# Performance work log

Measured on AMD Instinct MI355X. Metric: run time of the kernel, lower is better.

## Reference

```python
import jax, jax.numpy as jnp
import numpy as np

B, N, F_IN, F_OUT = 8, 2048, 128, 64
ALPHA = 0.2  # LeakyReLU negative slope
NEG_INF = -9e15


def setup_inputs() -> dict:
    key = jax.random.key(0)
    k1, k2, k3, k4 = jax.random.split(key, 4)
    h = jax.random.normal(k1, (B, N, F_IN), dtype=jnp.float32)
    adj = jax.random.randint(k2, (B, N, N), 0, 2, dtype=jnp.int32)
    # xavier_uniform with gain=1.414 approximated by scaled normals (values are arbitrary params)
    W = jax.random.normal(k3, (F_IN, F_OUT), dtype=jnp.float32) * (1.414 * np.sqrt(2.0 / (F_IN + F_OUT)))
    a = jax.random.normal(k4, (2 * F_OUT, 1), dtype=jnp.float32) * (1.414 * np.sqrt(2.0 / (2 * F_OUT + 1)))
    return {"h": h, "adj": adj, "W": W, "a": a}


def reference(h, adj, W, a):
    # Wh: [B, N, F_out]
    Wh = jnp.einsum('bnf,fo->bno', h, W)
    Fo = W.shape[1]
    a1 = a[:Fo, 0]   # [F_out]
    a2 = a[Fo:, 0]   # [F_out]
    # e[b,i,j] = leakyrelu(Wh[b,i]@a1 + Wh[b,j]@a2)  (== cat(Wh_i,Wh_j)@a, same math, no N^2*2F blowup)
    e1 = jnp.einsum('bno,o->bn', Wh, a1)  # [B, N]
    e2 = jnp.einsum('bno,o->bn', Wh, a2)  # [B, N]
    e = e1[:, :, None] + e2[:, None, :]   # [B, N, N]
    e = jnp.where(e > 0, e, ALPHA * e)    # LeakyReLU
    e = jnp.where(adj > 0, e, NEG_INF)    # mask non-edges
    attention = jax.nn.softmax(e, axis=-1)
    # dropout is identity in inference mode (deterministic reference)
    h_prime = jnp.einsum('bij,bjo->bio', attention, Wh)  # [B, N, F_out]
    return jax.nn.elu(h_prime)  # concat=True branch
```

## Files before the change

### kernel.cpp

```cpp
#include <hip/hip_runtime.h>
#include <hip/hip_bf16.h>

#define BB 8
#define NN 2048
#define FIN 128
#define FO 64
#define ALPHA 0.2f

typedef __attribute__((ext_vector_type(8))) short bf16x8;
typedef __attribute__((ext_vector_type(4))) float f32x4;
typedef __attribute__((ext_vector_type(4))) int i32x4;

typedef __attribute__((address_space(1))) const void gvoid;
typedef __attribute__((address_space(3))) void lvoid;

__device__ inline void gl_lds16(const void* g, void* l) {
    __builtin_amdgcn_global_load_lds((gvoid*)g, (lvoid*)l, 16, 0, 0);
}

__device__ inline short f2bf(float x) {
    unsigned u = __float_as_uint(x);
    u += 0x7fffu + ((u >> 16) & 1u);
    return (short)(u >> 16);
}

__global__ __launch_bounds__(256) void wh_kernel(
    const float* __restrict__ h, const float* __restrict__ W,
    const float* __restrict__ a, float* __restrict__ e1, float* __restrict__ e2,
    short* __restrict__ whF)
{
    __shared__ float hs[32][FIN];
    const int r0 = blockIdx.x * 32;
    const int t = threadIdx.x;
    const float4* hsrc = (const float4*)(h + (size_t)r0 * FIN);
    float4* hdst = (float4*)(&hs[0][0]);
#pragma unroll
    for (int k = 0; k < 4; k++) hdst[t + 256 * k] = hsrc[t + 256 * k];
    __syncthreads();

    const int o = t & 63;
    const int wv = t >> 6;
    float acc[8];
#pragma unroll
    for (int rr = 0; rr < 8; rr++) acc[rr] = 0.f;

    for (int f = 0; f < FIN; f += 4) {
        const float w0 = W[(f + 0) * FO + o];
        const float w1 = W[(f + 1) * FO + o];
        const float w2 = W[(f + 2) * FO + o];
        const float w3 = W[(f + 3) * FO + o];
#pragma unroll
        for (int rr = 0; rr < 8; rr++) {
            float4 hv = *(const float4*)&hs[wv * 8 + rr][f];
            acc[rr] = fmaf(hv.x, w0, acc[rr]);
            acc[rr] = fmaf(hv.y, w1, acc[rr]);
            acc[rr] = fmaf(hv.z, w2, acc[rr]);
            acc[rr] = fmaf(hv.w, w3, acc[rr]);
        }
    }

    const int b   = r0 / NN;
    const int ib0 = r0 - b * NN;
    const int ibb = ib0 + wv * 8;
    const int jc  = ibb >> 5;
    const int qq  = (ibb >> 3) & 3;
    const int ot  = o >> 4, mm = o & 15;
    const int L   = mm + qq * 16;
    bf16x8 frag;
#pragma unroll
    for (int rr = 0; rr < 8; rr++) frag[rr] = f2bf(acc[rr]);
    *(bf16x8*)(whF + ((((size_t)(b * 64 + jc) * 4 + ot) * 64 + L) * 8)) = frag;

    const float a1 = a[o], a2 = a[FO + o];
#pragma unroll
    for (int rr = 0; rr < 8; rr++) {
        float v1 = acc[rr] * a1, v2 = acc[rr] * a2;
#pragma unroll
        for (int msk = 32; msk >= 1; msk >>= 1) {
            v1 += __shfl_xor(v1, msk, 64);
            v2 += __shfl_xor(v2, msk, 64);
        }
        if (o == 0) { e1[r0 + wv * 8 + rr] = v1; e2[r0 + wv * 8 + rr] = v2; }
    }
}

__global__ __launch_bounds__(256) void e2max_kernel(
    const float* __restrict__ e2, float* __restrict__ e2max)
{
    const int b = blockIdx.x;
    const int t = threadIdx.x;
    float m = -1e30f;
    for (int j = t; j < NN; j += 256) m = fmaxf(m, e2[b * NN + j]);
#pragma unroll
    for (int k = 32; k >= 1; k >>= 1) m = fmaxf(m, __shfl_xor(m, k, 64));
    __shared__ float red[4];
    if ((t & 63) == 0) red[t >> 6] = m;
    __syncthreads();
    if (t == 0) e2max[b] = fmaxf(fmaxf(red[0], red[1]), fmaxf(red[2], red[3]));
}

struct SMemS { int adj[16][260]; float e2[256]; };
struct SMemC { float comb[4][16][64]; float lsum[4][16]; };
union SMemU { SMemS s; SMemC c; };

__global__ __launch_bounds__(256) void attn_kernel(
    const int* __restrict__ adj, const float* __restrict__ e1,
    const float* __restrict__ e2, const float* __restrict__ e2max,
    const short* __restrict__ whF, float* __restrict__ out)
{
    __shared__ SMemU sm;
    const int t = threadIdx.x, w = t >> 6, lane = t & 63;
    const int m = lane & 15, q = lane >> 4;
    const int blk = blockIdx.x;
    const int b  = blk >> 7;
    const int i0 = (blk & 127) * 16;
    const int i  = i0 + m;

    const float e1v = e1[b * NN + i];
    float mi = e1v + e2max[b];
    mi = mi > 0.f ? mi : ALPHA * mi;

    const short* whFb = whF + (size_t)b * (64 * 4 * 64 * 8);
    const int* arow0 = adj + ((size_t)(b * NN + i0)) * NN + lane * 4;
    const float* e2g = e2 + b * NN + lane * 4;

    f32x4 acc0 = {0.f,0.f,0.f,0.f}, acc1 = acc0, acc2 = acc0, acc3 = acc0;
    float lsum = 0.f;

    for (int j0 = 0; j0 < NN; j0 += 256) {
#pragma unroll
        for (int k = 0; k < 4; k++) {
            const int r = w * 4 + k;
            gl_lds16(arow0 + (size_t)r * NN + j0, &sm.s.adj[r][0]);
        }
        if (w == 0) gl_lds16(e2g + j0, &sm.s.e2[0]);
        __syncthreads();

#pragma unroll
        for (int s2 = 0; s2 < 2; s2++) {
            const int col = w * 64 + s2 * 32 + q * 8;
            i32x4 a0 = *(const i32x4*)&sm.s.adj[m][col];
            i32x4 a1 = *(const i32x4*)&sm.s.adj[m][col + 4];
            f32x4 ev0 = *(const f32x4*)&sm.s.e2[col];
            f32x4 ev1 = *(const f32x4*)&sm.s.e2[col + 4];

            bf16x8 af;
#pragma unroll
            for (int jj = 0; jj < 8; jj++) {
                const int   av  = (jj < 4) ? a0[jj]      : a1[jj - 4];
                const float e2j = (jj < 4) ? ev0[jj]     : ev1[jj - 4];
                float e = e1v + e2j;
                e = e > 0.f ? e : ALPHA * e;
                const float pe = (av > 0) ? __expf(e - mi) : 0.f;
                lsum += pe;
                af[jj] = f2bf(pe);
            }

            const int jc = (j0 + w * 64 + s2 * 32) >> 5;
            const short* bfp = whFb + (size_t)jc * 2048 + lane * 8;
            bf16x8 b0 = *(const bf16x8*)(bfp);
            bf16x8 b1 = *(const bf16x8*)(bfp + 512);
            bf16x8 b2 = *(const bf16x8*)(bfp + 1024);
            bf16x8 b3 = *(const bf16x8*)(bfp + 1536);

            acc0 = __builtin_amdgcn_mfma_f32_16x16x32_bf16(af, b0, acc0, 0, 0, 0);
            acc1 = __builtin_amdgcn_mfma_f32_16x16x32_bf16(af, b1, acc1, 0, 0, 0);
            acc2 = __builtin_amdgcn_mfma_f32_16x16x32_bf16(af, b2, acc2, 0, 0, 0);
            acc3 = __builtin_amdgcn_mfma_f32_16x16x32_bf16(af, b3, acc3, 0, 0, 0);
        }
        __syncthreads();
    }

    lsum += __shfl_xor(lsum, 16, 64);
    lsum += __shfl_xor(lsum, 32, 64);
    if (q == 0) sm.c.lsum[w][m] = lsum;
#pragma unroll
    for (int ot = 0; ot < 4; ot++) {
        f32x4 av = (ot == 0) ? acc0 : (ot == 1) ? acc1 : (ot == 2) ? acc2 : acc3;
#pragma unroll
        for (int reg = 0; reg < 4; reg++)
            sm.c.comb[w][q * 4 + reg][ot * 16 + m] = av[reg];
    }
    __syncthreads();

    const int row = t >> 4, c0 = (t & 15) * 4;
    f32x4 sum = *(const f32x4*)&sm.c.comb[0][row][c0];
#pragma unroll
    for (int ww = 1; ww < 4; ww++) {
        f32x4 sv = *(const f32x4*)&sm.c.comb[ww][row][c0];
        sum.x += sv.x; sum.y += sv.y; sum.z += sv.z; sum.w += sv.w;
    }
    float l = sm.c.lsum[0][row] + sm.c.lsum[1][row] + sm.c.lsum[2][row] + sm.c.lsum[3][row];
    l = fmaxf(l, 1e-30f);
    const float rl = 1.f / l;
    float vr[4] = { sum.x * rl, sum.y * rl, sum.z * rl, sum.w * rl };
    f32x4 res;
#pragma unroll
    for (int kk = 0; kk < 4; kk++)
        res[kk] = vr[kk] > 0.f ? vr[kk] : (__expf(vr[kk]) - 1.f);
    *(f32x4*)&out[((size_t)(b * NN + i0 + row)) * FO + c0] = res;
}

extern "C" void kernel_launch(void* const* d_in, const int* in_sizes, int n_in,
                              void* d_out, int out_size, void* d_ws, size_t ws_size,
                              hipStream_t stream) {
    const float* h   = (const float*)d_in[0];
    const int*   adj = (const int*)d_in[1];
    const float* W   = (const float*)d_in[2];
    const float* a   = (const float*)d_in[3];
    float* out = (float*)d_out;

    char* ws = (char*)d_ws;
    short* whF = (short*)ws;
    size_t off = (size_t)BB * 64 * 4 * 64 * 8 * sizeof(short);
    float* e1  = (float*)(ws + off);  off += (size_t)BB * NN * 4;
    float* e2  = (float*)(ws + off);  off += (size_t)BB * NN * 4;
    float* e2m = (float*)(ws + off);

    wh_kernel<<<(BB * NN) / 32, 256, 0, stream>>>(h, W, a, e1, e2, whF);
    e2max_kernel<<<BB, 256, 0, stream>>>(e2, e2m);
    attn_kernel<<<BB * (NN / 16), 256, 0, stream>>>(adj, e1, e2, e2m, whF, out);
}
```

Baseline: 216.6 us.

## Double-buffer adjacency tiles, prefetch operands to registers, fold e2 max into wh kernel

The attention kernel now double-buffers the adjacency tile in LDS and issues the next tile's global-to-LDS load before computing the current one, using manual vmcnt waits and raw barriers. The Wh fragments and e2 values are read straight into registers instead of staging e2 through LDS. The separate e2max reduction kernel is replaced by an order-preserving atomicMax in wh_kernel plus a tiny init kernel, and wh_kernel reads h directly from global instead of through LDS. This aims to hide adjacency load latency behind the exp/MFMA work. In exchange the hand-written waitcnt counts are fragile, and the extra LDS buffer plus the occupancy hint may affect occupancy.

```diff
diff --git a/kernel.cpp b/kernel.cpp
--- a/kernel.cpp
+++ b/kernel.cpp
@@ -24,22 +24,30 @@
     return (short)(u >> 16);
 }
 
+__device__ inline unsigned f2ord(float f) {
+    unsigned u = __float_as_uint(f);
+    return (u & 0x80000000u) ? ~u : (u | 0x80000000u);
+}
+__device__ inline float ord2f(unsigned v) {
+    return __uint_as_float((v & 0x80000000u) ? (v & 0x7fffffffu) : ~v);
+}
+
+__global__ void init_kernel(unsigned* __restrict__ e2m) {
+    if (threadIdx.x < BB) e2m[threadIdx.x] = 0u;
+}
+
 __global__ __launch_bounds__(256) void wh_kernel(
     const float* __restrict__ h, const float* __restrict__ W,
     const float* __restrict__ a, float* __restrict__ e1, float* __restrict__ e2,
-    short* __restrict__ whF)
+    unsigned* __restrict__ e2m, short* __restrict__ whF)
 {
-    __shared__ float hs[32][FIN];
+    const int t  = threadIdx.x;
+    const int o  = t & 63;
+    const int wv = t >> 6;
     const int r0 = blockIdx.x * 32;
-    const int t = threadIdx.x;
-    const float4* hsrc = (const float4*)(h + (size_t)r0 * FIN);
-    float4* hdst = (float4*)(&hs[0][0]);
-#pragma unroll
-    for (int k = 0; k < 4; k++) hdst[t + 256 * k] = hsrc[t + 256 * k];
-    __syncthreads();
-
-    const int o = t & 63;
-    const int wv = t >> 6;
+    const float* __restrict__ hrow =
+        h + (size_t)(r0 + __builtin_amdgcn_readfirstlane(wv) * 8) * FIN;
+
     float acc[8];
 #pragma unroll
     for (int rr = 0; rr < 8; rr++) acc[rr] = 0.f;
@@ -51,7 +59,7 @@
         const float w3 = W[(f + 3) * FO + o];
 #pragma unroll
         for (int rr = 0; rr < 8; rr++) {
-            float4 hv = *(const float4*)&hs[wv * 8 + rr][f];
+            const float4 hv = *(const float4*)(hrow + rr * FIN + f);
             acc[rr] = fmaf(hv.x, w0, acc[rr]);
             acc[rr] = fmaf(hv.y, w1, acc[rr]);
             acc[rr] = fmaf(hv.z, w2, acc[rr]);
@@ -72,6 +80,7 @@
     *(bf16x8*)(whF + ((((size_t)(b * 64 + jc) * 4 + ot) * 64 + L) * 8)) = frag;
 
     const float a1 = a[o], a2 = a[FO + o];
+    float vmax = -3.0e38f;
 #pragma unroll
     for (int rr = 0; rr < 8; rr++) {
         float v1 = acc[rr] * a1, v2 = acc[rr] * a2;
@@ -80,32 +89,19 @@
             v1 += __shfl_xor(v1, msk, 64);
             v2 += __shfl_xor(v2, msk, 64);
         }
+        vmax = fmaxf(vmax, v2);
         if (o == 0) { e1[r0 + wv * 8 + rr] = v1; e2[r0 + wv * 8 + rr] = v2; }
     }
-}
-
-__global__ __launch_bounds__(256) void e2max_kernel(
-    const float* __restrict__ e2, float* __restrict__ e2max)
-{
-    const int b = blockIdx.x;
-    const int t = threadIdx.x;
-    float m = -1e30f;
-    for (int j = t; j < NN; j += 256) m = fmaxf(m, e2[b * NN + j]);
-#pragma unroll
-    for (int k = 32; k >= 1; k >>= 1) m = fmaxf(m, __shfl_xor(m, k, 64));
-    __shared__ float red[4];
-    if ((t & 63) == 0) red[t >> 6] = m;
-    __syncthreads();
-    if (t == 0) e2max[b] = fmaxf(fmaxf(red[0], red[1]), fmaxf(red[2], red[3]));
-}
-
-struct SMemS { int adj[16][260]; float e2[256]; };
+    if (o == 0) atomicMax(&e2m[b], f2ord(vmax));
+}
+
+struct SMemS { int adj[2][16][260]; };
 struct SMemC { float comb[4][16][64]; float lsum[4][16]; };
-union SMemU { SMemS s; SMemC c; };
-
-__global__ __launch_bounds__(256) void attn_kernel(
+union __align__(16) SMemU { SMemS s; SMemC c; };
+
+__global__ __launch_bounds__(256, 4) void attn_kernel(
     const int* __restrict__ adj, const float* __restrict__ e1,
-    const float* __restrict__ e2, const float* __restrict__ e2max,
+    const float* __restrict__ e2, const unsigned* __restrict__ e2m,
     const short* __restrict__ whF, float* __restrict__ out)
 {
     __shared__ SMemU sm;
@@ -116,39 +112,71 @@
     const int i0 = (blk & 127) * 16;
     const int i  = i0 + m;
 
+    const float e2mx = ord2f(e2m[b]);
     const float e1v = e1[b * NN + i];
-    float mi = e1v + e2max[b];
+    float mi = e1v + e2mx;
     mi = mi > 0.f ? mi : ALPHA * mi;
 
     const short* whFb = whF + (size_t)b * (64 * 4 * 64 * 8);
     const int* arow0 = adj + ((size_t)(b * NN + i0)) * NN + lane * 4;
-    const float* e2g = e2 + b * NN + lane * 4;
+    const float* e2b = e2 + b * NN;
 
     f32x4 acc0 = {0.f,0.f,0.f,0.f}, acc1 = acc0, acc2 = acc0, acc3 = acc0;
     float lsum = 0.f;
 
-    for (int j0 = 0; j0 < NN; j0 += 256) {
-#pragma unroll
-        for (int k = 0; k < 4; k++) {
-            const int r = w * 4 + k;
-            gl_lds16(arow0 + (size_t)r * NN + j0, &sm.s.adj[r][0]);
-        }
-        if (w == 0) gl_lds16(e2g + j0, &sm.s.e2[0]);
-        __syncthreads();
+#pragma unroll
+    for (int k = 0; k < 4; k++)
+        gl_lds16(arow0 + (size_t)(w * 4 + k) * NN, &sm.s.adj[0][w * 4 + k][0]);
+
+#pragma unroll 2
+    for (int tt = 0; tt < 8; tt++) {
+        const int j0 = tt * 256;
+        const int cb = tt & 1;
+
+        const short* bfpA = whFb + (size_t)((j0 + w * 64) >> 5) * 2048 + lane * 8;
+        bf16x8 b00 = *(const bf16x8*)(bfpA);
+        bf16x8 b01 = *(const bf16x8*)(bfpA + 512);
+        bf16x8 b02 = *(const bf16x8*)(bfpA + 1024);
+        bf16x8 b03 = *(const bf16x8*)(bfpA + 1536);
+        const short* bfpB = bfpA + 2048;
+        bf16x8 b10 = *(const bf16x8*)(bfpB);
+        bf16x8 b11 = *(const bf16x8*)(bfpB + 512);
+        bf16x8 b12 = *(const bf16x8*)(bfpB + 1024);
+        bf16x8 b13 = *(const bf16x8*)(bfpB + 1536);
+
+        const float* e2w = e2b + j0 + w * 64 + q * 8;
+        f32x4 ev00 = *(const f32x4*)(e2w);
+        f32x4 ev01 = *(const f32x4*)(e2w + 4);
+        f32x4 ev10 = *(const f32x4*)(e2w + 32);
+        f32x4 ev11 = *(const f32x4*)(e2w + 36);
+
+        asm volatile("" ::: "memory");
+
+        if (tt < 7) {
+            const int jn = j0 + 256;
+#pragma unroll
+            for (int k = 0; k < 4; k++)
+                gl_lds16(arow0 + (size_t)(w * 4 + k) * NN + jn,
+                         &sm.s.adj[cb ^ 1][w * 4 + k][0]);
+            asm volatile("s_waitcnt vmcnt(16)" ::: "memory");
+        } else {
+            asm volatile("s_waitcnt vmcnt(12)" ::: "memory");
+        }
+        __builtin_amdgcn_s_barrier();
 
 #pragma unroll
         for (int s2 = 0; s2 < 2; s2++) {
             const int col = w * 64 + s2 * 32 + q * 8;
-            i32x4 a0 = *(const i32x4*)&sm.s.adj[m][col];
-            i32x4 a1 = *(const i32x4*)&sm.s.adj[m][col + 4];
-            f32x4 ev0 = *(const f32x4*)&sm.s.e2[col];
-            f32x4 ev1 = *(const f32x4*)&sm.s.e2[col + 4];
+            i32x4 a0 = *(const i32x4*)&sm.s.adj[cb][m][col];
+            i32x4 a1 = *(const i32x4*)&sm.s.adj[cb][m][col + 4];
+            const f32x4 ev0 = s2 ? ev10 : ev00;
+            const f32x4 ev1 = s2 ? ev11 : ev01;
 
             bf16x8 af;
 #pragma unroll
             for (int jj = 0; jj < 8; jj++) {
-                const int   av  = (jj < 4) ? a0[jj]      : a1[jj - 4];
-                const float e2j = (jj < 4) ? ev0[jj]     : ev1[jj - 4];
+                const int   av  = (jj < 4) ? a0[jj]  : a1[jj - 4];
+                const float e2j = (jj < 4) ? ev0[jj] : ev1[jj - 4];
                 float e = e1v + e2j;
                 e = e > 0.f ? e : ALPHA * e;
                 const float pe = (av > 0) ? __expf(e - mi) : 0.f;
@@ -156,19 +184,20 @@
                 af[jj] = f2bf(pe);
             }
 
-            const int jc = (j0 + w * 64 + s2 * 32) >> 5;
-            const short* bfp = whFb + (size_t)jc * 2048 + lane * 8;
-            bf16x8 b0 = *(const bf16x8*)(bfp);
-            bf16x8 b1 = *(const bf16x8*)(bfp + 512);
-            bf16x8 b2 = *(const bf16x8*)(bfp + 1024);
-            bf16x8 b3 = *(const bf16x8*)(bfp + 1536);
-
-            acc0 = __builtin_amdgcn_mfma_f32_16x16x32_bf16(af, b0, acc0, 0, 0, 0);
-            acc1 = __builtin_amdgcn_mfma_f32_16x16x32_bf16(af, b1, acc1, 0, 0, 0);
-            acc2 = __builtin_amdgcn_mfma_f32_16x16x32_bf16(af, b2, acc2, 0, 0, 0);
-            acc3 = __builtin_amdgcn_mfma_f32_16x16x32_bf16(af, b3, acc3, 0, 0, 0);
-        }
-        __syncthreads();
+            if (s2 == 0) {
+                acc0 = __builtin_amdgcn_mfma_f32_16x16x32_bf16(af, b00, acc0, 0, 0, 0);
+                acc1 = __builtin_amdgcn_mfma_f32_16x16x32_bf16(af, b01, acc1, 0, 0, 0);
+                acc2 = __builtin_amdgcn_mfma_f32_16x16x32_bf16(af, b02, acc2, 0, 0, 0);
+                acc3 = __builtin_amdgcn_mfma_f32_16x16x32_bf16(af, b03, acc3, 0, 0, 0);
+            } else {
+                acc0 = __builtin_amdgcn_mfma_f32_16x16x32_bf16(af, b10, acc0, 0, 0, 0);
+                acc1 = __builtin_amdgcn_mfma_f32_16x16x32_bf16(af, b11, acc1, 0, 0, 0);
+                acc2 = __builtin_amdgcn_mfma_f32_16x16x32_bf16(af, b12, acc2, 0, 0, 0);
+                acc3 = __builtin_amdgcn_mfma_f32_16x16x32_bf16(af, b13, acc3, 0, 0, 0);
+            }
+        }
+        asm volatile("s_waitcnt lgkmcnt(0)" ::: "memory");
+        __builtin_amdgcn_s_barrier();
     }
 
     lsum += __shfl_xor(lsum, 16, 64);
@@ -215,9 +244,9 @@
     size_t off = (size_t)BB * 64 * 4 * 64 * 8 * sizeof(short);
     float* e1  = (float*)(ws + off);  off += (size_t)BB * NN * 4;
     float* e2  = (float*)(ws + off);  off += (size_t)BB * NN * 4;
-    float* e2m = (float*)(ws + off);
-
-    wh_kernel<<<(BB * NN) / 32, 256, 0, stream>>>(h, W, a, e1, e2, whF);
-    e2max_kernel<<<BB, 256, 0, stream>>>(e2, e2m);
+    unsigned* e2m = (unsigned*)(ws + off);
+
+    init_kernel<<<1, 64, 0, stream>>>(e2m);
+    wh_kernel<<<(BB * NN) / 32, 256, 0, stream>>>(h, W, a, e1, e2, e2m, whF);
     attn_kernel<<<BB * (NN / 16), 256, 0, stream>>>(adj, e1, e2, e2m, whF, out);
 }
```

After: 246.6 us. +13.9%, slower.

## Split attention over two column halves, fold e2 max into projection kernel

Applied to the files above, without the earlier changes.

The attention kernel now splits each 16-row tile's 2048 neighbour columns into two halves, launching twice as many blocks. Each block writes partial accumulators and row sums to workspace, and a new combine kernel merges the halves and applies normalization and ELU. The separate e2max kernel is removed: wh_kernel writes per-wave partial maxima, and each attention block reduces these itself. wh_kernel also reads h directly from global memory instead of staging it in LDS. The goal is more parallelism, fewer launches and less LDS traffic, at the cost of extra partial-result memory traffic and an additional kernel launch.

```diff
diff --git a/kernel.cpp b/kernel.cpp
--- a/kernel.cpp
+++ b/kernel.cpp
@@ -27,19 +27,15 @@
 __global__ __launch_bounds__(256) void wh_kernel(
     const float* __restrict__ h, const float* __restrict__ W,
     const float* __restrict__ a, float* __restrict__ e1, float* __restrict__ e2,
-    short* __restrict__ whF)
+    float* __restrict__ e2p, short* __restrict__ whF)
 {
-    __shared__ float hs[32][FIN];
+    const int t  = threadIdx.x;
+    const int o  = t & 63;
+    const int wv = t >> 6;
     const int r0 = blockIdx.x * 32;
-    const int t = threadIdx.x;
-    const float4* hsrc = (const float4*)(h + (size_t)r0 * FIN);
-    float4* hdst = (float4*)(&hs[0][0]);
-#pragma unroll
-    for (int k = 0; k < 4; k++) hdst[t + 256 * k] = hsrc[t + 256 * k];
-    __syncthreads();
-
-    const int o = t & 63;
-    const int wv = t >> 6;
+    const float* __restrict__ hrow =
+        h + (size_t)(r0 + __builtin_amdgcn_readfirstlane(wv) * 8) * FIN;
+
     float acc[8];
 #pragma unroll
     for (int rr = 0; rr < 8; rr++) acc[rr] = 0.f;
@@ -51,7 +47,7 @@
         const float w3 = W[(f + 3) * FO + o];
 #pragma unroll
         for (int rr = 0; rr < 8; rr++) {
-            float4 hv = *(const float4*)&hs[wv * 8 + rr][f];
+            const float4 hv = *(const float4*)(hrow + rr * FIN + f);
             acc[rr] = fmaf(hv.x, w0, acc[rr]);
             acc[rr] = fmaf(hv.y, w1, acc[rr]);
             acc[rr] = fmaf(hv.z, w2, acc[rr]);
@@ -72,6 +68,7 @@
     *(bf16x8*)(whF + ((((size_t)(b * 64 + jc) * 4 + ot) * 64 + L) * 8)) = frag;
 
     const float a1 = a[o], a2 = a[FO + o];
+    float vmax = -3.0e38f;
 #pragma unroll
     for (int rr = 0; rr < 8; rr++) {
         float v1 = acc[rr] * a1, v2 = acc[rr] * a2;
@@ -80,54 +77,54 @@
             v1 += __shfl_xor(v1, msk, 64);
             v2 += __shfl_xor(v2, msk, 64);
         }
+        vmax = fmaxf(vmax, v2);
         if (o == 0) { e1[r0 + wv * 8 + rr] = v1; e2[r0 + wv * 8 + rr] = v2; }
     }
-}
-
-__global__ __launch_bounds__(256) void e2max_kernel(
-    const float* __restrict__ e2, float* __restrict__ e2max)
-{
-    const int b = blockIdx.x;
-    const int t = threadIdx.x;
-    float m = -1e30f;
-    for (int j = t; j < NN; j += 256) m = fmaxf(m, e2[b * NN + j]);
-#pragma unroll
-    for (int k = 32; k >= 1; k >>= 1) m = fmaxf(m, __shfl_xor(m, k, 64));
-    __shared__ float red[4];
-    if ((t & 63) == 0) red[t >> 6] = m;
-    __syncthreads();
-    if (t == 0) e2max[b] = fmaxf(fmaxf(red[0], red[1]), fmaxf(red[2], red[3]));
+    if (o == 0) e2p[b * 256 + (ib0 >> 5) * 4 + wv] = vmax;
 }
 
 struct SMemS { int adj[16][260]; float e2[256]; };
 struct SMemC { float comb[4][16][64]; float lsum[4][16]; };
-union SMemU { SMemS s; SMemC c; };
-
-__global__ __launch_bounds__(256) void attn_kernel(
+union __align__(16) SMemU { SMemS s; SMemC c; };
+
+__global__ __launch_bounds__(256, 8) void attn_kernel(
     const int* __restrict__ adj, const float* __restrict__ e1,
-    const float* __restrict__ e2, const float* __restrict__ e2max,
-    const short* __restrict__ whF, float* __restrict__ out)
+    const float* __restrict__ e2, const float* __restrict__ e2p,
+    const short* __restrict__ whF, float* __restrict__ pacc,
+    float* __restrict__ plsum)
 {
     __shared__ SMemU sm;
+    __shared__ float red4[4];
     const int t = threadIdx.x, w = t >> 6, lane = t & 63;
     const int m = lane & 15, q = lane >> 4;
     const int blk = blockIdx.x;
-    const int b  = blk >> 7;
-    const int i0 = (blk & 127) * 16;
-    const int i  = i0 + m;
-
+    const int jh  = blk >> 10;
+    const int tb  = blk & 1023;
+    const int b   = tb >> 7;
+    const int i0  = (tb & 127) * 16;
+    const int i   = i0 + m;
+
+    float pv = e2p[b * 256 + t];
     const float e1v = e1[b * NN + i];
-    float mi = e1v + e2max[b];
+#pragma unroll
+    for (int k = 32; k >= 1; k >>= 1) pv = fmaxf(pv, __shfl_xor(pv, k, 64));
+    if (lane == 0) red4[w] = pv;
+    __syncthreads();
+    const float e2mx = fmaxf(fmaxf(red4[0], red4[1]), fmaxf(red4[2], red4[3]));
+
+    float mi = e1v + e2mx;
     mi = mi > 0.f ? mi : ALPHA * mi;
 
     const short* whFb = whF + (size_t)b * (64 * 4 * 64 * 8);
     const int* arow0 = adj + ((size_t)(b * NN + i0)) * NN + lane * 4;
     const float* e2g = e2 + b * NN + lane * 4;
+    const int jbase = jh * 1024;
 
     f32x4 acc0 = {0.f,0.f,0.f,0.f}, acc1 = acc0, acc2 = acc0, acc3 = acc0;
     float lsum = 0.f;
 
-    for (int j0 = 0; j0 < NN; j0 += 256) {
+    for (int tt = 0; tt < 4; tt++) {
+        const int j0 = jbase + tt * 256;
 #pragma unroll
         for (int k = 0; k < 4; k++) {
             const int r = w * 4 + k;
@@ -190,14 +187,34 @@
         f32x4 sv = *(const f32x4*)&sm.c.comb[ww][row][c0];
         sum.x += sv.x; sum.y += sv.y; sum.z += sv.z; sum.w += sv.w;
     }
-    float l = sm.c.lsum[0][row] + sm.c.lsum[1][row] + sm.c.lsum[2][row] + sm.c.lsum[3][row];
+    *(f32x4*)&pacc[((size_t)blk * 16 + row) * 64 + c0] = sum;
+    if ((t & 15) == 0) {
+        plsum[blk * 16 + row] = sm.c.lsum[0][row] + sm.c.lsum[1][row]
+                              + sm.c.lsum[2][row] + sm.c.lsum[3][row];
+    }
+}
+
+__global__ __launch_bounds__(256) void comb_kernel(
+    const float* __restrict__ pacc, const float* __restrict__ plsum,
+    float* __restrict__ out)
+{
+    const int tb = blockIdx.x;
+    const int t = threadIdx.x;
+    const int row = t >> 4, c0 = (t & 15) * 4;
+    const int b = tb >> 7;
+    const int i0 = (tb & 127) * 16;
+
+    f32x4 s0 = *(const f32x4*)&pacc[((size_t)tb * 16 + row) * 64 + c0];
+    f32x4 s1 = *(const f32x4*)&pacc[((size_t)(1024 + tb) * 16 + row) * 64 + c0];
+    float l = plsum[tb * 16 + row] + plsum[(1024 + tb) * 16 + row];
     l = fmaxf(l, 1e-30f);
     const float rl = 1.f / l;
-    float vr[4] = { sum.x * rl, sum.y * rl, sum.z * rl, sum.w * rl };
     f32x4 res;
 #pragma unroll
-    for (int kk = 0; kk < 4; kk++)
-        res[kk] = vr[kk] > 0.f ? vr[kk] : (__expf(vr[kk]) - 1.f);
+    for (int k = 0; k < 4; k++) {
+        const float v = (s0[k] + s1[k]) * rl;
+        res[k] = v > 0.f ? v : (__expf(v) - 1.f);
+    }
     *(f32x4*)&out[((size_t)(b * NN + i0 + row)) * FO + c0] = res;
 }
 
@@ -215,9 +232,11 @@
     size_t off = (size_t)BB * 64 * 4 * 64 * 8 * sizeof(short);
     float* e1  = (float*)(ws + off);  off += (size_t)BB * NN * 4;
     float* e2  = (float*)(ws + off);  off += (size_t)BB * NN * 4;
-    float* e2m = (float*)(ws + off);
-
-    wh_kernel<<<(BB * NN) / 32, 256, 0, stream>>>(h, W, a, e1, e2, whF);
-    e2max_kernel<<<BB, 256, 0, stream>>>(e2, e2m);
-    attn_kernel<<<BB * (NN / 16), 256, 0, stream>>>(adj, e1, e2, e2m, whF, out);
-}
+    float* e2p = (float*)(ws + off);  off += (size_t)BB * 256 * 4;
+    float* pacc  = (float*)(ws + off); off += (size_t)2048 * 16 * 64 * 4;
+    float* plsum = (float*)(ws + off);
+
+    wh_kernel<<<(BB * NN) / 32, 256, 0, stream>>>(h, W, a, e1, e2, e2p, whF);
+    attn_kernel<<<2048, 256, 0, stream>>>(adj, e1, e2, e2p, whF, pacc, plsum);
+    comb_kernel<<<1024, 256, 0, stream>>>(pacc, plsum, out);
+}
```

Result: slower. 257.3 us (+18.8%).
